# Optimization experiments

Hardware: AMD Instinct MI355X
Metric: run time of the kernel (lower is better)

Reference implementation:

```python
import jax, jax.numpy as jnp
import numpy as np

N, E, F, EB, NB, G = 50000, 800000, 64, 20, 3, 100
CUTOFF = 5.0
NUM_EMB = 119


def silu(x):
    return x * jax.nn.sigmoid(x)


def setup_inputs() -> dict:
    key = jax.random.key(0)
    ks = jax.random.split(key, 16)
    w = lambda k, shape, scale: jax.random.normal(k, shape, dtype=jnp.float32) * scale
    inp = {}
    # forward args
    inp["node_features"] = jax.random.randint(ks[0], (N,), 1, NUM_EMB)
    inp["node_positions"] = jax.random.normal(ks[1], (N, 3), dtype=jnp.float32)
    inp["edge_index"] = jax.random.randint(ks[2], (2, E), 0, N)
    inp["node_graph_index"] = jnp.sort(jax.random.randint(ks[3], (N,), 0, G))
    # learned parameters (stacked over NB interaction blocks)
    inp["emb"] = w(ks[4], (NUM_EMB, F), 1.0)
    inp["msg_W1"] = w(ks[5], (NB, F, F), F ** -0.5)
    inp["msg_b1"] = jnp.zeros((NB, F), jnp.float32)
    inp["msg_W2"] = w(ks[6], (NB, F, 3 * F), F ** -0.5)
    inp["msg_b2"] = jnp.zeros((NB, 3 * F), jnp.float32)
    inp["filt_W"] = w(ks[7], (NB, EB, 3 * F), EB ** -0.5)
    inp["filt_b"] = jnp.zeros((NB, 3 * F), jnp.float32)
    inp["upd_U"] = w(ks[8], (NB, F, F), F ** -0.5)
    inp["upd_V"] = w(ks[9], (NB, F, F), F ** -0.5)
    inp["upd_W1"] = w(ks[10], (NB, 2 * F, F), (2 * F) ** -0.5)
    inp["upd_b1"] = jnp.zeros((NB, F), jnp.float32)
    inp["upd_W2"] = w(ks[11], (NB, F, 3 * F), F ** -0.5)
    inp["upd_b2"] = jnp.zeros((NB, 3 * F), jnp.float32)
    # readout MLP: Linear(F,F) + SiLU + Linear(F,1)
    inp["ro_W1"] = w(ks[12], (F, F), F ** -0.5)
    inp["ro_b1"] = jnp.zeros((F,), jnp.float32)
    inp["ro_W2"] = w(ks[13], (F, 1), F ** -0.5)
    inp["ro_b2"] = jnp.zeros((1,), jnp.float32)
    return inp


def _painn_forward(node_positions, emb, msg_W1, msg_b1, msg_W2, msg_b2,
                   filt_W, filt_b, upd_U, upd_V, upd_W1, upd_b1, upd_W2, upd_b2,
                   ro_W1, ro_b1, ro_W2, ro_b2,
                   node_features, edge_index, node_graph_index):
    recv, send = edge_index[0], edge_index[1]  # row aggregates over col neighbors
    s = emb[node_features]                      # [N,F] scalar node states
    v = jnp.zeros((N, 3, F), s.dtype)           # [N,3,F] vector node states

    # edge geometry
    d = node_positions[send] - node_positions[recv]       # [E,3]
    r = jnp.sqrt(jnp.sum(d * d, axis=1, keepdims=True))   # [E,1]
    dhat = d / (r + 1e-10)                                # unit edge vectors

    # Bessel (sinc) radial basis expansion of edge norms: [E,EB]
    n = jnp.arange(1, EB + 1, dtype=s.dtype)
    rbf = jnp.sqrt(2.0 / CUTOFF) * jnp.sin(n * jnp.pi * r / CUTOFF) / (r + 1e-10)
    # smooth cosine cutoff: [E,1]
    fc = jnp.where(r < CUTOFF, 0.5 * (jnp.cos(jnp.pi * r / CUTOFF) + 1.0), 0.0)

    for b in range(NB):
        # --- message block ---
        phi = silu(s @ msg_W1[b] + msg_b1[b]) @ msg_W2[b] + msg_b2[b]   # [N,3F]
        Wf = (rbf @ filt_W[b] + filt_b[b]) * fc                          # [E,3F]
        m = phi[send] * Wf                                               # [E,3F]
        gate_v, gate_e, m_s = jnp.split(m, 3, axis=-1)                   # [E,F] each
        m_v = v[send] * gate_v[:, None, :] + dhat[:, :, None] * gate_e[:, None, :]  # [E,3,F]
        s = s + jax.ops.segment_sum(m_s, recv, num_segments=N)
        v = v + jax.ops.segment_sum(m_v, recv, num_segments=N)
        # --- update block ---
        Uv = jnp.einsum('ndf,fg->ndg', v, upd_U[b])                      # [N,3,F]
        Vv = jnp.einsum('ndf,fg->ndg', v, upd_V[b])                      # [N,3,F]
        Vn = jnp.sqrt(jnp.sum(Vv * Vv, axis=1) + 1e-8)                   # [N,F]
        a = silu(jnp.concatenate([s, Vn], axis=-1) @ upd_W1[b] + upd_b1[b]) @ upd_W2[b] + upd_b2[b]
        a_vv, a_sv, a_ss = jnp.split(a, 3, axis=-1)
        v = v + a_vv[:, None, :] * Uv
        s = s + a_sv * jnp.sum(Uv * Vv, axis=1) + a_ss

    # readout MLP + per-graph sum reduction
    ro = silu(s @ ro_W1 + ro_b1) @ ro_W2 + ro_b2                         # [N,1]
    graph_out = jax.ops.segment_sum(ro, node_graph_index, num_segments=G)  # [G,1]

    # graph Laplacian of final scalar states
    deg = jax.ops.segment_sum(jnp.ones((E,), s.dtype), recv, num_segments=N)  # [N]
    lap = deg[:, None] * s - jax.ops.segment_sum(s[send], recv, num_segments=N)  # [N,F]
    return graph_out, s, lap


def reference(node_features, node_positions, edge_index, node_graph_index,
              emb, msg_W1, msg_b1, msg_W2, msg_b2, filt_W, filt_b,
              upd_U, upd_V, upd_W1, upd_b1, upd_W2, upd_b2,
              ro_W1, ro_b1, ro_W2, ro_b2):
    return _painn_forward(node_positions, emb, msg_W1, msg_b1, msg_W2, msg_b2,
                          filt_W, filt_b, upd_U, upd_V, upd_W1, upd_b1, upd_W2, upd_b2,
                          ro_W1, ro_b1, ro_W2, ro_b2,
                          node_features, edge_index, node_graph_index)
```

## Files before the change

### kernel.cpp

```cpp
#include <hip/hip_runtime.h>

#define NN 50000
#define NE 800000
#define FF 64
#define EB 20
#define NBLK 3
#define NG 100

__device__ __forceinline__ float silu_f(float x) {
  return x / (1.f + expf(-x));
}

__global__ __launch_bounds__(256) void k_init(float4* v0, int* cnt, float* gout) {
  int i = blockIdx.x * blockDim.x + threadIdx.x;
  if (i < NN * 48) v0[i] = make_float4(0.f, 0.f, 0.f, 0.f);
  if (i < NN) cnt[i] = 0;
  if (i < NG) gout[i] = 0.f;
}

__global__ __launch_bounds__(256) void k_embed(const int* __restrict__ feat,
                                               const float* __restrict__ emb,
                                               const int* __restrict__ ei,
                                               float* __restrict__ s, int* cnt) {
  int i = blockIdx.x * blockDim.x + threadIdx.x;
  if (i < NN * FF) s[i] = emb[feat[i >> 6] * FF + (i & 63)];
  if (i < NE) atomicAdd(&cnt[ei[i]], 1);
}

__global__ __launch_bounds__(1024) void k_scan(const int* __restrict__ cnt,
                                               int* __restrict__ rowst,
                                               int* __restrict__ rowcur) {
  __shared__ int part[1024];
  int t = threadIdx.x;
  const int CH = 52;
  int base = t * CH;
  int own = 0;
  const int4* c4 = (const int4*)(cnt + base);
#pragma unroll
  for (int i = 0; i < CH / 4; i++) {
    int idx = base + i * 4;
    if (idx + 3 < NN) {
      int4 q = c4[i];
      own += q.x + q.y + q.z + q.w;
    } else {
      for (int j = 0; j < 4; j++)
        if (idx + j < NN) own += cnt[idx + j];
    }
  }
  part[t] = own;
  __syncthreads();
  for (int off = 1; off < 1024; off <<= 1) {
    int v = (t >= off) ? part[t - off] : 0;
    __syncthreads();
    part[t] += v;
    __syncthreads();
  }
  int excl = part[t] - own;
  for (int i = 0; i < CH; i++) {
    int idx = base + i;
    if (idx < NN) {
      rowst[idx] = excl;
      rowcur[idx] = excl;
      excl += cnt[idx];
    }
  }
  if (t == 1023) rowst[NN] = excl;
}

__global__ __launch_bounds__(256) void k_fillgeo(const int* __restrict__ ei,
                                                 const float* __restrict__ pos,
                                                 int* rowcur, float4* __restrict__ d4,
                                                 int* __restrict__ eid) {
  int e = blockIdx.x * blockDim.x + threadIdx.x;
  if (e >= NE) return;
  int rv = ei[e], sd = ei[NE + e];
  float dx = pos[sd * 3 + 0] - pos[rv * 3 + 0];
  float dy = pos[sd * 3 + 1] - pos[rv * 3 + 1];
  float dz = pos[sd * 3 + 2] - pos[rv * 3 + 2];
  float r = sqrtf(dx * dx + dy * dy + dz * dz);
  d4[e] = make_float4(dx, dy, dz, r);
  int slot = atomicAdd(&rowcur[rv], 1);
  eid[slot] = e;
}

__global__ __launch_bounds__(256) void k_rbf(const int* __restrict__ ei,
                                             const float4* __restrict__ d4,
                                             const int* __restrict__ eid,
                                             float4* __restrict__ geo,
                                             int* __restrict__ send_s,
                                             float* __restrict__ rbf2) {
  __shared__ float buf[256 * EB];
  int tid = threadIdx.x;
  int slot = blockIdx.x * 256 + tid;
  int e = eid[slot];
  float4 d = d4[e];
  float r = d.w;
  float inv = 1.f / (r + 1e-10f);
  float fc = (r < 5.0f) ? 0.5f * (cosf(0.6283185307179586f * r) + 1.f) : 0.f;
  geo[slot] = make_float4(d.x * inv, d.y * inv, d.z * inv, fc);
  send_s[slot] = ei[NE + e];
  float cs = 0.6324555320336759f * inv * fc;
#pragma unroll
  for (int k = 0; k < EB; k++)
    buf[tid * EB + k] = cs * sinf((float)(k + 1) * 0.6283185307179586f * r);
  __syncthreads();
  size_t base = (size_t)blockIdx.x * 256 * EB;
#pragma unroll
  for (int i = 0; i < EB; i++)
    rbf2[base + i * 256 + tid] = buf[i * 256 + tid];
}

__global__ __launch_bounds__(256) void k_phi1(const float* __restrict__ s,
                                              const float* __restrict__ W1,
                                              const float* __restrict__ b1,
                                              float* __restrict__ h) {
  int lane = threadIdx.x & 63;
  int gw = (blockIdx.x * blockDim.x + threadIdx.x) >> 6;
  int nw = (gridDim.x * blockDim.x) >> 6;
  float w[FF];
#pragma unroll
  for (int k = 0; k < FF; k++) w[k] = W1[k * FF + lane];
  float bb = b1[lane];
  for (int n0 = gw; n0 < NN; n0 += nw) {
    int n = __builtin_amdgcn_readfirstlane(n0);
    const float4* row = (const float4*)(s + (size_t)n * FF);
    float a0 = bb, a1 = 0.f, a2 = 0.f, a3 = 0.f;
#pragma unroll
    for (int q = 0; q < 16; q++) {
      float4 x = row[q];
      a0 = fmaf(x.x, w[4 * q], a0);
      a1 = fmaf(x.y, w[4 * q + 1], a1);
      a2 = fmaf(x.z, w[4 * q + 2], a2);
      a3 = fmaf(x.w, w[4 * q + 3], a3);
    }
    h[(size_t)n * FF + lane] = silu_f((a0 + a1) + (a2 + a3));
  }
}

__global__ __launch_bounds__(256) void k_phi2(const float* __restrict__ h,
                                              const float* __restrict__ W2,
                                              const float* __restrict__ b2,
                                              float3* __restrict__ phi3) {
  int lane = threadIdx.x & 63;
  int gw = (blockIdx.x * blockDim.x + threadIdx.x) >> 6;
  int nw = (gridDim.x * blockDim.x) >> 6;
  float w0[FF], w1[FF], w2[FF];
#pragma unroll
  for (int k = 0; k < FF; k++) {
    w0[k] = W2[k * 192 + lane];
    w1[k] = W2[k * 192 + 64 + lane];
    w2[k] = W2[k * 192 + 128 + lane];
  }
  float c0 = b2[lane], c1 = b2[64 + lane], c2 = b2[128 + lane];
  for (int n0 = gw; n0 < NN; n0 += nw) {
    int n = __builtin_amdgcn_readfirstlane(n0);
    const float4* row = (const float4*)(h + (size_t)n * FF);
    float a0 = c0, a1 = c1, a2 = c2;
#pragma unroll
    for (int q = 0; q < 16; q++) {
      float4 x = row[q];
      a0 = fmaf(x.x, w0[4 * q], a0);
      a1 = fmaf(x.x, w1[4 * q], a1);
      a2 = fmaf(x.x, w2[4 * q], a2);
      a0 = fmaf(x.y, w0[4 * q + 1], a0);
      a1 = fmaf(x.y, w1[4 * q + 1], a1);
      a2 = fmaf(x.y, w2[4 * q + 1], a2);
      a0 = fmaf(x.z, w0[4 * q + 2], a0);
      a1 = fmaf(x.z, w1[4 * q + 2], a1);
      a2 = fmaf(x.z, w2[4 * q + 2], a2);
      a0 = fmaf(x.w, w0[4 * q + 3], a0);
      a1 = fmaf(x.w, w1[4 * q + 3], a1);
      a2 = fmaf(x.w, w2[4 * q + 3], a2);
    }
    phi3[(size_t)n * FF + lane] = make_float3(a0, a1, a2);
  }
}

template <bool FIRST>
__global__ __launch_bounds__(256) void k_msg(const float3* __restrict__ phi3,
                                             const float3* __restrict__ v03,
                                             float* __restrict__ s,
                                             float3* __restrict__ v13,
                                             const float* __restrict__ fW,
                                             const float* __restrict__ fb,
                                             const float4* __restrict__ geo,
                                             const int* __restrict__ send_s,
                                             const int* __restrict__ rowst,
                                             const float* __restrict__ rbf2) {
  int lane = threadIdx.x & 63;
  int gw = (blockIdx.x * blockDim.x + threadIdx.x) >> 6;
  int nw = (gridDim.x * blockDim.x) >> 6;
  float fw0[EB], fw1[EB], fw2[EB];
#pragma unroll
  for (int k = 0; k < EB; k++) {
    fw0[k] = fW[k * 192 + lane];
    fw1[k] = fW[k * 192 + 64 + lane];
    fw2[k] = fW[k * 192 + 128 + lane];
  }
  float fb0 = fb[lane], fb1 = fb[64 + lane], fb2 = fb[128 + lane];
  for (int n0 = gw; n0 < NN; n0 += nw) {
    int n = __builtin_amdgcn_readfirstlane(n0);
    int beg = rowst[n], end = rowst[n + 1];
    float accs = 0.f, av0 = 0.f, av1 = 0.f, av2 = 0.f;
    for (int slot = beg; slot < end; slot++) {
      float4 g = geo[slot];
      if (g.w > 0.f) {
        int j = send_s[slot];
        const float4* rp = (const float4*)(rbf2 + (size_t)slot * EB);
        float4 q0 = rp[0], q1 = rp[1], q2 = rp[2], q3 = rp[3], q4 = rp[4];
        float rb[EB] = {q0.x, q0.y, q0.z, q0.w, q1.x, q1.y, q1.z, q1.w,
                        q2.x, q2.y, q2.z, q2.w, q3.x, q3.y, q3.z, q3.w,
                        q4.x, q4.y, q4.z, q4.w};
        float wf1 = fb1 * g.w, wf2 = fb2 * g.w;
#pragma unroll
        for (int k = 0; k < EB; k++) {
          wf1 = fmaf(rb[k], fw1[k], wf1);
          wf2 = fmaf(rb[k], fw2[k], wf2);
        }
        float3 pj = phi3[(size_t)j * FF + lane];
        float ge = pj.y * wf1;
        accs = fmaf(pj.z, wf2, accs);
        if (!FIRST) {
          float wf0 = fb0 * g.w;
#pragma unroll
          for (int k = 0; k < EB; k++) wf0 = fmaf(rb[k], fw0[k], wf0);
          float gv = pj.x * wf0;
          float3 vj = v03[(size_t)j * FF + lane];
          av0 = fmaf(vj.x, gv, fmaf(g.x, ge, av0));
          av1 = fmaf(vj.y, gv, fmaf(g.y, ge, av1));
          av2 = fmaf(vj.z, gv, fmaf(g.z, ge, av2));
        } else {
          av0 = fmaf(g.x, ge, av0);
          av1 = fmaf(g.y, ge, av1);
          av2 = fmaf(g.z, ge, av2);
        }
      }
    }
    s[(size_t)n * FF + lane] += accs;
    if (!FIRST) {
      float3 vo = v03[(size_t)n * FF + lane];
      v13[(size_t)n * FF + lane] =
          make_float3(vo.x + av0, vo.y + av1, vo.z + av2);
    } else {
      v13[(size_t)n * FF + lane] = make_float3(av0, av1, av2);
    }
  }
}

__global__ __launch_bounds__(256) void k_upd1(const float3* __restrict__ v13,
                                              const float* __restrict__ U,
                                              const float* __restrict__ V,
                                              float3* __restrict__ Uv3,
                                              float* __restrict__ Vn,
                                              float* __restrict__ dotUV) {
  int lane = threadIdx.x & 63;
  int gw = (blockIdx.x * blockDim.x + threadIdx.x) >> 6;
  int nw = (gridDim.x * blockDim.x) >> 6;
  float u[FF], w[FF];
#pragma unroll
  for (int k = 0; k < FF; k++) {
    u[k] = U[k * FF + lane];
    w[k] = V[k * FF + lane];
  }
  for (int n0 = gw; n0 < NN; n0 += nw) {
    int n = __builtin_amdgcn_readfirstlane(n0);
    const float4* row = (const float4*)((const float*)v13 + (size_t)n * 192);
    float uv0 = 0, uv1 = 0, uv2 = 0, vv0 = 0, vv1 = 0, vv2 = 0;
#pragma unroll
    for (int gq = 0; gq < 16; gq++) {
      float4 A = row[3 * gq], B = row[3 * gq + 1], C = row[3 * gq + 2];
      int k = 4 * gq;
      uv0 = fmaf(A.x, u[k], uv0); vv0 = fmaf(A.x, w[k], vv0);
      uv1 = fmaf(A.y, u[k], uv1); vv1 = fmaf(A.y, w[k], vv1);
      uv2 = fmaf(A.z, u[k], uv2); vv2 = fmaf(A.z, w[k], vv2);
      uv0 = fmaf(A.w, u[k + 1], uv0); vv0 = fmaf(A.w, w[k + 1], vv0);
      uv1 = fmaf(B.x, u[k + 1], uv1); vv1 = fmaf(B.x, w[k + 1], vv1);
      uv2 = fmaf(B.y, u[k + 1], uv2); vv2 = fmaf(B.y, w[k + 1], vv2);
      uv0 = fmaf(B.z, u[k + 2], uv0); vv0 = fmaf(B.z, w[k + 2], vv0);
      uv1 = fmaf(B.w, u[k + 2], uv1); vv1 = fmaf(B.w, w[k + 2], vv1);
      uv2 = fmaf(C.x, u[k + 2], uv2); vv2 = fmaf(C.x, w[k + 2], vv2);
      uv0 = fmaf(C.y, u[k + 3], uv0); vv0 = fmaf(C.y, w[k + 3], vv0);
      uv1 = fmaf(C.z, u[k + 3], uv1); vv1 = fmaf(C.z, w[k + 3], vv1);
      uv2 = fmaf(C.w, u[k + 3], uv2); vv2 = fmaf(C.w, w[k + 3], vv2);
    }
    Uv3[(size_t)n * FF + lane] = make_float3(uv0, uv1, uv2);
    Vn[(size_t)n * FF + lane] = sqrtf(vv0 * vv0 + vv1 * vv1 + vv2 * vv2 + 1e-8f);
    dotUV[(size_t)n * FF + lane] = uv0 * vv0 + uv1 * vv1 + uv2 * vv2;
  }
}

__global__ __launch_bounds__(256) void k_upd2(const float* __restrict__ s,
                                              const float* __restrict__ Vn,
                                              const float* __restrict__ W1,
                                              const float* __restrict__ b1,
                                              float* __restrict__ h) {
  int lane = threadIdx.x & 63;
  int gw = (blockIdx.x * blockDim.x + threadIdx.x) >> 6;
  int nw = (gridDim.x * blockDim.x) >> 6;
  float w[2 * FF];
#pragma unroll
  for (int k = 0; k < 2 * FF; k++) w[k] = W1[k * FF + lane];
  float bb = b1[lane];
  for (int n0 = gw; n0 < NN; n0 += nw) {
    int n = __builtin_amdgcn_readfirstlane(n0);
    const float4* rs = (const float4*)(s + (size_t)n * FF);
    const float4* rv = (const float4*)(Vn + (size_t)n * FF);
    float a0 = bb, a1 = 0.f, a2 = 0.f, a3 = 0.f;
#pragma unroll
    for (int q = 0; q < 16; q++) {
      float4 x = rs[q];
      a0 = fmaf(x.x, w[4 * q], a0);
      a1 = fmaf(x.y, w[4 * q + 1], a1);
      a2 = fmaf(x.z, w[4 * q + 2], a2);
      a3 = fmaf(x.w, w[4 * q + 3], a3);
    }
#pragma unroll
    for (int q = 0; q < 16; q++) {
      float4 x = rv[q];
      a0 = fmaf(x.x, w[FF + 4 * q], a0);
      a1 = fmaf(x.y, w[FF + 4 * q + 1], a1);
      a2 = fmaf(x.z, w[FF + 4 * q + 2], a2);
      a3 = fmaf(x.w, w[FF + 4 * q + 3], a3);
    }
    h[(size_t)n * FF + lane] = silu_f((a0 + a1) + (a2 + a3));
  }
}

__global__ __launch_bounds__(256) void k_upd3(const float* __restrict__ h,
                                              const float* __restrict__ W2,
                                              const float* __restrict__ b2,
                                              const float3* __restrict__ Uv3,
                                              const float3* __restrict__ v13,
                                              const float* __restrict__ dotUV,
                                              float3* __restrict__ v03,
                                              float* __restrict__ s) {
  int lane = threadIdx.x & 63;
  int gw = (blockIdx.x * blockDim.x + threadIdx.x) >> 6;
  int nw = (gridDim.x * blockDim.x) >> 6;
  float w0[FF], w1[FF], w2[FF];
#pragma unroll
  for (int k = 0; k < FF; k++) {
    w0[k] = W2[k * 192 + lane];
    w1[k] = W2[k * 192 + 64 + lane];
    w2[k] = W2[k * 192 + 128 + lane];
  }
  float c0 = b2[lane], c1 = b2[64 + lane], c2 = b2[128 + lane];
  for (int n0 = gw; n0 < NN; n0 += nw) {
    int n = __builtin_amdgcn_readfirstlane(n0);
    const float4* row = (const float4*)(h + (size_t)n * FF);
    float a0 = c0, a1 = c1, a2 = c2;
#pragma unroll
    for (int q = 0; q < 16; q++) {
      float4 x = row[q];
      a0 = fmaf(x.x, w0[4 * q], a0);
      a1 = fmaf(x.x, w1[4 * q], a1);
      a2 = fmaf(x.x, w2[4 * q], a2);
      a0 = fmaf(x.y, w0[4 * q + 1], a0);
      a1 = fmaf(x.y, w1[4 * q + 1], a1);
      a2 = fmaf(x.y, w2[4 * q + 1], a2);
      a0 = fmaf(x.z, w0[4 * q + 2], a0);
      a1 = fmaf(x.z, w1[4 * q + 2], a1);
      a2 = fmaf(x.z, w2[4 * q + 2], a2);
      a0 = fmaf(x.w, w0[4 * q + 3], a0);
      a1 = fmaf(x.w, w1[4 * q + 3], a1);
      a2 = fmaf(x.w, w2[4 * q + 3], a2);
    }
    float3 uv = Uv3[(size_t)n * FF + lane];
    float3 vv = v13[(size_t)n * FF + lane];
    v03[(size_t)n * FF + lane] = make_float3(
        fmaf(a0, uv.x, vv.x), fmaf(a0, uv.y, vv.y), fmaf(a0, uv.z, vv.z));
    size_t i_ = (size_t)n * FF + lane;
    s[i_] = fmaf(a1, dotUV[i_], s[i_] + a2);
  }
}

__global__ __launch_bounds__(256) void k_final(const float* __restrict__ s,
                                               const float* __restrict__ roW1,
                                               const float* __restrict__ rob1,
                                               const float* __restrict__ roW2,
                                               const float* __restrict__ rob2,
                                               const int* __restrict__ gidx,
                                               const int* __restrict__ rowst,
                                               const int* __restrict__ send_s,
                                               float* __restrict__ gout,
                                               float* __restrict__ lap) {
  int lane = threadIdx.x & 63;
  int gw = (blockIdx.x * blockDim.x + threadIdx.x) >> 6;
  int nw = (gridDim.x * blockDim.x) >> 6;
  float w[FF];
#pragma unroll
  for (int k = 0; k < FF; k++) w[k] = roW1[k * FF + lane];
  float b1v = rob1[lane], w2v = roW2[lane], b2v = rob2[0];
  for (int n0 = gw; n0 < NN; n0 += nw) {
    int n = __builtin_amdgcn_readfirstlane(n0);
    int beg = rowst[n], end = rowst[n + 1];
    float acc = 0.f;
    for (int slot = beg; slot < end; slot++) {
      int j = send_s[slot];
      acc += s[(size_t)j * FF + lane];
    }
    float sv = s[(size_t)n * FF + lane];
    lap[(size_t)n * FF + lane] = (float)(end - beg) * sv - acc;
    const float4* row = (const float4*)(s + (size_t)n * FF);
    float a0 = b1v, a1 = 0.f, a2 = 0.f, a3 = 0.f;
#pragma unroll
    for (int q = 0; q < 16; q++) {
      float4 x = row[q];
      a0 = fmaf(x.x, w[4 * q], a0);
      a1 = fmaf(x.y, w[4 * q + 1], a1);
      a2 = fmaf(x.z, w[4 * q + 2], a2);
      a3 = fmaf(x.w, w[4 * q + 3], a3);
    }
    float c = silu_f((a0 + a1) + (a2 + a3)) * w2v;
#pragma unroll
    for (int off = 32; off > 0; off >>= 1) c += __shfl_down(c, off, 64);
    if (lane == 0) atomicAdd(&gout[gidx[n]], c + b2v);
  }
}

extern "C" void kernel_launch(void* const* d_in, const int* in_sizes, int n_in,
                              void* d_out, int out_size, void* d_ws, size_t ws_size,
                              hipStream_t stream) {
  const int* feat = (const int*)d_in[0];
  const float* pos = (const float*)d_in[1];
  const int* ei = (const int*)d_in[2];
  const int* gidx = (const int*)d_in[3];
  const float* emb = (const float*)d_in[4];
  const float* msgW1 = (const float*)d_in[5];
  const float* msgb1 = (const float*)d_in[6];
  const float* msgW2 = (const float*)d_in[7];
  const float* msgb2 = (const float*)d_in[8];
  const float* filtW = (const float*)d_in[9];
  const float* filtb = (const float*)d_in[10];
  const float* updU = (const float*)d_in[11];
  const float* updV = (const float*)d_in[12];
  const float* updW1 = (const float*)d_in[13];
  const float* updb1 = (const float*)d_in[14];
  const float* updW2 = (const float*)d_in[15];
  const float* updb2 = (const float*)d_in[16];
  const float* roW1 = (const float*)d_in[17];
  const float* rob1 = (const float*)d_in[18];
  const float* roW2 = (const float*)d_in[19];
  const float* rob2 = (const float*)d_in[20];

  float* gout = (float*)d_out;
  float* s = gout + NG;
  float* lap = s + (size_t)NN * FF;

  char* p = (char*)d_ws;
  auto alloc = [&](size_t bytes) {
    char* r = p;
    p += (bytes + 255) & ~(size_t)255;
    return r;
  };
  float3* v03 = (float3*)alloc((size_t)NN * 192 * 4);
  float3* v13 = (float3*)alloc((size_t)NN * 192 * 4);
  float3* phiUv3 = (float3*)alloc((size_t)NN * 192 * 4);
  float* h = (float*)alloc((size_t)NN * FF * 4);
  float* Vn = (float*)alloc((size_t)NN * FF * 4);
  float* dotUV = (float*)alloc((size_t)NN * FF * 4);
  float4* geo = (float4*)alloc((size_t)NE * 16);
  float4* d4 = (float4*)alloc((size_t)NE * 16);
  float* rbf2 = (float*)alloc((size_t)NE * EB * 4);
  int* send_s = (int*)alloc((size_t)NE * 4);
  int* eid = (int*)alloc((size_t)NE * 4);
  int* rowst = (int*)alloc((size_t)(NN + 1) * 4);
  int* rowcur = (int*)alloc((size_t)NN * 4);
  int* cnt = (int*)alloc((size_t)NN * 4);

  k_init<<<(NN * 48 + 255) / 256, 256, 0, stream>>>((float4*)v03, cnt, gout);
  k_embed<<<(NN * FF + 255) / 256, 256, 0, stream>>>(feat, emb, ei, s, cnt);
  k_scan<<<1, 1024, 0, stream>>>(cnt, rowst, rowcur);
  k_fillgeo<<<NE / 256, 256, 0, stream>>>(ei, pos, rowcur, d4, eid);
  k_rbf<<<NE / 256, 256, 0, stream>>>(ei, d4, eid, geo, send_s, rbf2);

  for (int b = 0; b < NBLK; b++) {
    k_phi1<<<1024, 256, 0, stream>>>(s, msgW1 + b * FF * FF, msgb1 + b * FF, h);
    k_phi2<<<1024, 256, 0, stream>>>(h, msgW2 + b * FF * 192, msgb2 + b * 192,
                                     phiUv3);
    if (b == 0)
      k_msg<true><<<2048, 256, 0, stream>>>(phiUv3, v03, s, v13,
                                            filtW + b * EB * 192,
                                            filtb + b * 192, geo, send_s,
                                            rowst, rbf2);
    else
      k_msg<false><<<2048, 256, 0, stream>>>(phiUv3, v03, s, v13,
                                             filtW + b * EB * 192,
                                             filtb + b * 192, geo, send_s,
                                             rowst, rbf2);
    k_upd1<<<1024, 256, 0, stream>>>(v13, updU + b * FF * FF, updV + b * FF * FF,
                                     phiUv3, Vn, dotUV);
    k_upd2<<<1024, 256, 0, stream>>>(s, Vn, updW1 + b * 2 * FF * FF,
                                     updb1 + b * FF, h);
    k_upd3<<<1024, 256, 0, stream>>>(h, updW2 + b * FF * 192, updb2 + b * 192,
                                     phiUv3, v13, dotUV, v03, s);
  }

  k_final<<<2048, 256, 0, stream>>>(s, roW1, rob1, roW2, rob2, gidx, rowst,
                                    send_s, gout, lap);
}
```

Before: 2.170 ms.

## Batch neighbor gathers with readlane broadcast and pack edge records

The message kernel now loads up to 64 sender indices per wave at once and broadcasts them with readlane. It processes four edges per iteration, so several phi/v gathers are in flight together, and it reads a packed 24-float per-edge record (RBF, unit direction, cutoff) with one coalesced lane load plus readlane broadcasts. The Laplacian gather in the final kernel uses the same batched-index scheme with eight independent accumulators. Grid sizes are doubled for most kernels. Edges outside the cutoff are no longer skipped, which adds some wasted work in exchange for the added memory-level parallelism.

Result: faster. 2.047 ms (-5.7%).

```diff
diff --git a/kernel.cpp b/kernel.cpp
--- a/kernel.cpp
+++ b/kernel.cpp
@@ -4,9 +4,13 @@
 #define NE 800000
 #define FF 64
 #define EB 20
+#define REC 24
 #define NBLK 3
 #define NG 100
 
+__device__ __forceinline__ float bcastf(float v, int k) {
+  return __int_as_float(__builtin_amdgcn_readlane(__float_as_int(v), k));
+}
 __device__ __forceinline__ float silu_f(float x) {
   return x / (1.f + expf(-x));
 }
@@ -86,10 +90,9 @@
 __global__ __launch_bounds__(256) void k_rbf(const int* __restrict__ ei,
                                              const float4* __restrict__ d4,
                                              const int* __restrict__ eid,
-                                             float4* __restrict__ geo,
-                                             int* __restrict__ send_s,
-                                             float* __restrict__ rbf2) {
-  __shared__ float buf[256 * EB];
+                                             float* __restrict__ rec,
+                                             int* __restrict__ send_s) {
+  __shared__ float buf[256 * REC];
   int tid = threadIdx.x;
   int slot = blockIdx.x * 256 + tid;
   int e = eid[slot];
@@ -97,17 +100,20 @@
   float r = d.w;
   float inv = 1.f / (r + 1e-10f);
   float fc = (r < 5.0f) ? 0.5f * (cosf(0.6283185307179586f * r) + 1.f) : 0.f;
-  geo[slot] = make_float4(d.x * inv, d.y * inv, d.z * inv, fc);
   send_s[slot] = ei[NE + e];
   float cs = 0.6324555320336759f * inv * fc;
 #pragma unroll
   for (int k = 0; k < EB; k++)
-    buf[tid * EB + k] = cs * sinf((float)(k + 1) * 0.6283185307179586f * r);
+    buf[tid * REC + k] = cs * sinf((float)(k + 1) * 0.6283185307179586f * r);
+  buf[tid * REC + 20] = d.x * inv;
+  buf[tid * REC + 21] = d.y * inv;
+  buf[tid * REC + 22] = d.z * inv;
+  buf[tid * REC + 23] = fc;
   __syncthreads();
-  size_t base = (size_t)blockIdx.x * 256 * EB;
-#pragma unroll
-  for (int i = 0; i < EB; i++)
-    rbf2[base + i * 256 + tid] = buf[i * 256 + tid];
+  size_t base = (size_t)blockIdx.x * 256 * REC;
+#pragma unroll
+  for (int i = 0; i < REC; i++)
+    rec[base + i * 256 + tid] = buf[i * 256 + tid];
 }
 
 __global__ __launch_bounds__(256) void k_phi1(const float* __restrict__ s,
@@ -183,17 +189,16 @@
                                              float3* __restrict__ v13,
                                              const float* __restrict__ fW,
                                              const float* __restrict__ fb,
-                                             const float4* __restrict__ geo,
+                                             const float* __restrict__ rec,
                                              const int* __restrict__ send_s,
-                                             const int* __restrict__ rowst,
-                                             const float* __restrict__ rbf2) {
+                                             const int* __restrict__ rowst) {
   int lane = threadIdx.x & 63;
   int gw = (blockIdx.x * blockDim.x + threadIdx.x) >> 6;
   int nw = (gridDim.x * blockDim.x) >> 6;
   float fw0[EB], fw1[EB], fw2[EB];
 #pragma unroll
   for (int k = 0; k < EB; k++) {
-    fw0[k] = fW[k * 192 + lane];
+    if (!FIRST) fw0[k] = fW[k * 192 + lane];
     fw1[k] = fW[k * 192 + 64 + lane];
     fw2[k] = fW[k * 192 + 128 + lane];
   }
@@ -202,39 +207,72 @@
     int n = __builtin_amdgcn_readfirstlane(n0);
     int beg = rowst[n], end = rowst[n + 1];
     float accs = 0.f, av0 = 0.f, av1 = 0.f, av2 = 0.f;
-    for (int slot = beg; slot < end; slot++) {
-      float4 g = geo[slot];
-      if (g.w > 0.f) {
-        int j = send_s[slot];
-        const float4* rp = (const float4*)(rbf2 + (size_t)slot * EB);
-        float4 q0 = rp[0], q1 = rp[1], q2 = rp[2], q3 = rp[3], q4 = rp[4];
-        float rb[EB] = {q0.x, q0.y, q0.z, q0.w, q1.x, q1.y, q1.z, q1.w,
-                        q2.x, q2.y, q2.z, q2.w, q3.x, q3.y, q3.z, q3.w,
-                        q4.x, q4.y, q4.z, q4.w};
-        float wf1 = fb1 * g.w, wf2 = fb2 * g.w;
-#pragma unroll
-        for (int k = 0; k < EB; k++) {
-          wf1 = fmaf(rb[k], fw1[k], wf1);
-          wf2 = fmaf(rb[k], fw2[k], wf2);
+    for (int base = beg; base < end; base += 64) {
+      int cnt = end - base;
+      if (cnt > 64) cnt = 64;
+      int jl = (base + lane < end) ? send_s[base + lane] : 0;
+      int t = 0;
+      for (; t + 4 <= cnt; t += 4) {
+        size_t s0 = base + t, s1 = s0 + 1, s2 = s0 + 2, s3 = s0 + 3;
+        int j0 = __builtin_amdgcn_readlane(jl, t);
+        int j1 = __builtin_amdgcn_readlane(jl, t + 1);
+        int j2 = __builtin_amdgcn_readlane(jl, t + 2);
+        int j3 = __builtin_amdgcn_readlane(jl, t + 3);
+        float r0 = (lane < REC) ? rec[s0 * REC + lane] : 0.f;
+        float r1 = (lane < REC) ? rec[s1 * REC + lane] : 0.f;
+        float r2 = (lane < REC) ? rec[s2 * REC + lane] : 0.f;
+        float r3 = (lane < REC) ? rec[s3 * REC + lane] : 0.f;
+        float3 p0 = phi3[(size_t)j0 * FF + lane];
+        float3 p1 = phi3[(size_t)j1 * FF + lane];
+        float3 p2 = phi3[(size_t)j2 * FF + lane];
+        float3 p3 = phi3[(size_t)j3 * FF + lane];
+        float3 v0, v1, v2, v3;
+        if (!FIRST) {
+          v0 = v03[(size_t)j0 * FF + lane];
+          v1 = v03[(size_t)j1 * FF + lane];
+          v2 = v03[(size_t)j2 * FF + lane];
+          v3 = v03[(size_t)j3 * FF + lane];
         }
-        float3 pj = phi3[(size_t)j * FF + lane];
-        float ge = pj.y * wf1;
-        accs = fmaf(pj.z, wf2, accs);
-        if (!FIRST) {
-          float wf0 = fb0 * g.w;
-#pragma unroll
-          for (int k = 0; k < EB; k++) wf0 = fmaf(rb[k], fw0[k], wf0);
-          float gv = pj.x * wf0;
-          float3 vj = v03[(size_t)j * FF + lane];
-          av0 = fmaf(vj.x, gv, fmaf(g.x, ge, av0));
-          av1 = fmaf(vj.y, gv, fmaf(g.y, ge, av1));
-          av2 = fmaf(vj.z, gv, fmaf(g.z, ge, av2));
-        } else {
-          av0 = fmaf(g.x, ge, av0);
-          av1 = fmaf(g.y, ge, av1);
-          av2 = fmaf(g.z, ge, av2);
+#define SLOT(ri, pi, vi)                                                    \
+        {                                                                   \
+          float fc = bcastf(ri, 23);                                        \
+          float gx = bcastf(ri, 20), gy = bcastf(ri, 21), gz = bcastf(ri, 22); \
+          float wf0 = fb0 * fc, wf1 = fb1 * fc, wf2 = fb2 * fc;             \
+          _Pragma("unroll")                                                 \
+          for (int k = 0; k < EB; k++) {                                    \
+            float rk = bcastf(ri, k);                                       \
+            if (!FIRST) wf0 = fmaf(rk, fw0[k], wf0);                        \
+            wf1 = fmaf(rk, fw1[k], wf1);                                    \
+            wf2 = fmaf(rk, fw2[k], wf2);                                    \
+          }                                                                 \
+          float ge = pi.y * wf1;                                            \
+          accs = fmaf(pi.z, wf2, accs);                                     \
+          if (!FIRST) {                                                     \
+            float gv = pi.x * wf0;                                          \
+            av0 = fmaf(vi.x, gv, fmaf(gx, ge, av0));                        \
+            av1 = fmaf(vi.y, gv, fmaf(gy, ge, av1));                        \
+            av2 = fmaf(vi.z, gv, fmaf(gz, ge, av2));                        \
+          } else {                                                          \
+            av0 = fmaf(gx, ge, av0);                                        \
+            av1 = fmaf(gy, ge, av1);                                        \
+            av2 = fmaf(gz, ge, av2);                                        \
+          }                                                                 \
         }
+        SLOT(r0, p0, v0)
+        SLOT(r1, p1, v1)
+        SLOT(r2, p2, v2)
+        SLOT(r3, p3, v3)
       }
+      for (; t < cnt; t++) {
+        size_t s0 = base + t;
+        int j0 = __builtin_amdgcn_readlane(jl, t);
+        float r0 = (lane < REC) ? rec[s0 * REC + lane] : 0.f;
+        float3 p0 = phi3[(size_t)j0 * FF + lane];
+        float3 v0;
+        if (!FIRST) v0 = v03[(size_t)j0 * FF + lane];
+        SLOT(r0, p0, v0)
+      }
+#undef SLOT
     }
     s[(size_t)n * FF + lane] += accs;
     if (!FIRST) {
@@ -394,11 +432,37 @@
   for (int n0 = gw; n0 < NN; n0 += nw) {
     int n = __builtin_amdgcn_readfirstlane(n0);
     int beg = rowst[n], end = rowst[n + 1];
-    float acc = 0.f;
-    for (int slot = beg; slot < end; slot++) {
-      int j = send_s[slot];
-      acc += s[(size_t)j * FF + lane];
-    }
+    float ac0 = 0.f, ac1 = 0.f, ac2 = 0.f, ac3 = 0.f;
+    float ac4 = 0.f, ac5 = 0.f, ac6 = 0.f, ac7 = 0.f;
+    for (int base = beg; base < end; base += 64) {
+      int cnt = end - base;
+      if (cnt > 64) cnt = 64;
+      int jl = (base + lane < end) ? send_s[base + lane] : 0;
+      int t = 0;
+      for (; t + 8 <= cnt; t += 8) {
+        int j0 = __builtin_amdgcn_readlane(jl, t);
+        int j1 = __builtin_amdgcn_readlane(jl, t + 1);
+        int j2 = __builtin_amdgcn_readlane(jl, t + 2);
+        int j3 = __builtin_amdgcn_readlane(jl, t + 3);
+        int j4 = __builtin_amdgcn_readlane(jl, t + 4);
+        int j5 = __builtin_amdgcn_readlane(jl, t + 5);
+        int j6 = __builtin_amdgcn_readlane(jl, t + 6);
+        int j7 = __builtin_amdgcn_readlane(jl, t + 7);
+        ac0 += s[(size_t)j0 * FF + lane];
+        ac1 += s[(size_t)j1 * FF + lane];
+        ac2 += s[(size_t)j2 * FF + lane];
+        ac3 += s[(size_t)j3 * FF + lane];
+        ac4 += s[(size_t)j4 * FF + lane];
+        ac5 += s[(size_t)j5 * FF + lane];
+        ac6 += s[(size_t)j6 * FF + lane];
+        ac7 += s[(size_t)j7 * FF + lane];
+      }
+      for (; t < cnt; t++) {
+        int j0 = __builtin_amdgcn_readlane(jl, t);
+        ac0 += s[(size_t)j0 * FF + lane];
+      }
+    }
+    float acc = ((ac0 + ac1) + (ac2 + ac3)) + ((ac4 + ac5) + (ac6 + ac7));
     float sv = s[(size_t)n * FF + lane];
     lap[(size_t)n * FF + lane] = (float)(end - beg) * sv - acc;
     const float4* row = (const float4*)(s + (size_t)n * FF);
@@ -459,9 +523,8 @@
   float* h = (float*)alloc((size_t)NN * FF * 4);
   float* Vn = (float*)alloc((size_t)NN * FF * 4);
   float* dotUV = (float*)alloc((size_t)NN * FF * 4);
-  float4* geo = (float4*)alloc((size_t)NE * 16);
+  float* rec = (float*)alloc((size_t)NE * REC * 4);
   float4* d4 = (float4*)alloc((size_t)NE * 16);
-  float* rbf2 = (float*)alloc((size_t)NE * EB * 4);
   int* send_s = (int*)alloc((size_t)NE * 4);
   int* eid = (int*)alloc((size_t)NE * 4);
   int* rowst = (int*)alloc((size_t)(NN + 1) * 4);
@@ -472,30 +535,30 @@
   k_embed<<<(NN * FF + 255) / 256, 256, 0, stream>>>(feat, emb, ei, s, cnt);
   k_scan<<<1, 1024, 0, stream>>>(cnt, rowst, rowcur);
   k_fillgeo<<<NE / 256, 256, 0, stream>>>(ei, pos, rowcur, d4, eid);
-  k_rbf<<<NE / 256, 256, 0, stream>>>(ei, d4, eid, geo, send_s, rbf2);
+  k_rbf<<<NE / 256, 256, 0, stream>>>(ei, d4, eid, rec, send_s);
 
   for (int b = 0; b < NBLK; b++) {
-    k_phi1<<<1024, 256, 0, stream>>>(s, msgW1 + b * FF * FF, msgb1 + b * FF, h);
-    k_phi2<<<1024, 256, 0, stream>>>(h, msgW2 + b * FF * 192, msgb2 + b * 192,
+    k_phi1<<<2048, 256, 0, stream>>>(s, msgW1 + b * FF * FF, msgb1 + b * FF, h);
+    k_phi2<<<2048, 256, 0, stream>>>(h, msgW2 + b * FF * 192, msgb2 + b * 192,
                                      phiUv3);
     if (b == 0)
-      k_msg<true><<<2048, 256, 0, stream>>>(phiUv3, v03, s, v13,
+      k_msg<true><<<4096, 256, 0, stream>>>(phiUv3, v03, s, v13,
                                             filtW + b * EB * 192,
-                                            filtb + b * 192, geo, send_s,
-                                            rowst, rbf2);
+                                            filtb + b * 192, rec, send_s,
+                                            rowst);
     else
-      k_msg<false><<<2048, 256, 0, stream>>>(phiUv3, v03, s, v13,
+      k_msg<false><<<4096, 256, 0, stream>>>(phiUv3, v03, s, v13,
                                              filtW + b * EB * 192,
-                                             filtb + b * 192, geo, send_s,
-                                             rowst, rbf2);
-    k_upd1<<<1024, 256, 0, stream>>>(v13, updU + b * FF * FF, updV + b * FF * FF,
+                                             filtb + b * 192, rec, send_s,
+                                             rowst);
+    k_upd1<<<2048, 256, 0, stream>>>(v13, updU + b * FF * FF, updV + b * FF * FF,
                                      phiUv3, Vn, dotUV);
-    k_upd2<<<1024, 256, 0, stream>>>(s, Vn, updW1 + b * 2 * FF * FF,
+    k_upd2<<<2048, 256, 0, stream>>>(s, Vn, updW1 + b * 2 * FF * FF,
                                      updb1 + b * FF, h);
-    k_upd3<<<1024, 256, 0, stream>>>(h, updW2 + b * FF * 192, updb2 + b * 192,
+    k_upd3<<<2048, 256, 0, stream>>>(h, updW2 + b * FF * 192, updb2 + b * 192,
                                      phiUv3, v13, dotUV, v03, s);
   }
 
-  k_final<<<2048, 256, 0, stream>>>(s, roW1, rob1, roW2, rob2, gidx, rowst,
+  k_final<<<4096, 256, 0, stream>>>(s, roW1, rob1, roW2, rob2, gidx, rowst,
                                     send_s, gout, lap);
 }
```
